# Optimization experiments

Hardware: AMD Instinct MI355X
Metric: run time of the kernel (lower is better)

The kernel has to match this reference:

```python
import jax, jax.numpy as jnp
import numpy as np
from jax import lax

K = 10
ALPHA = 0.1
N_NODES = 100000
N_EDGES = 3200000


def setup_inputs() -> dict:
    key = jax.random.key(0)
    ks = jax.random.split(key, 6)
    x = jax.random.normal(ks[0], (N_NODES, 256), dtype=jnp.float32)
    edge_index = jax.random.randint(ks[1], (2, N_EDGES), 0, N_NODES, dtype=jnp.int64)
    w1 = jax.random.normal(ks[2], (256, 256), dtype=jnp.float32) * (1.0 / np.sqrt(256))
    b1 = jax.random.normal(ks[3], (256,), dtype=jnp.float32) * 0.01
    w2 = jax.random.normal(ks[4], (64, 256), dtype=jnp.float32) * (1.0 / np.sqrt(256))
    b2 = jax.random.normal(ks[5], (64,), dtype=jnp.float32) * 0.01
    return {"x": x, "edge_index": edge_index, "w1": w1, "b1": b1, "w2": w2, "b2": b2}


def reference(x, edge_index, w1, b1, w2, b2):
    # Eval mode: dropout is identity.
    h = jax.nn.relu(x @ w1.T + b1)          # [N, hidden]
    z = h @ w2.T + b2                        # [N, out]

    n = x.shape[0]
    loop = jnp.arange(n, dtype=edge_index.dtype)
    row = jnp.concatenate([edge_index[0], loop])   # sources (with self-loops)
    col = jnp.concatenate([edge_index[1], loop])   # targets (with self-loops)

    # gcn_norm: D^{-1/2} (A + I) D^{-1/2}, degree at target nodes
    deg = jax.ops.segment_sum(jnp.ones_like(col, dtype=z.dtype), col, num_segments=n)
    dinv = lax.rsqrt(deg)                    # deg >= 1 due to self-loops
    norm = dinv[row] * dinv[col]             # [E+N]

    x0 = z

    def step(xk, _):
        msg = xk[row] * norm[:, None]                          # gather + scale
        agg = jax.ops.segment_sum(msg, col, num_segments=n)    # scatter-add
        return (1.0 - ALPHA) * agg + ALPHA * x0, None

    out, _ = lax.scan(step, z, None, length=K)
    return out
```

## Files before the change

### kernel.cpp

```cpp
#include <hip/hip_runtime.h>
#include <hip/hip_bf16.h>


#define HIDDEN 256
#define OUTF   64
#define NB_BLK 256

typedef __attribute__((ext_vector_type(8))) unsigned short ushort8;
typedef __attribute__((ext_vector_type(8))) short short8v;
typedef __attribute__((ext_vector_type(4))) float f32x4;

__device__ inline float b2f(unsigned short u) {
    union { unsigned int i; float f; } c;
    c.i = ((unsigned int)u) << 16;
    return c.f;
}
__device__ inline unsigned short f2b(float f) {
    union { float f; unsigned int i; } c;
    c.f = f;
    unsigned int x = c.i;
    unsigned int r = (x + 0x7fff + ((x >> 16) & 1)) >> 16;
    return (unsigned short)r;
}
__device__ inline short8v cvt8v(float4 A, float4 B) {
    short8v o;
    o[0] = (short)f2b(A.x); o[1] = (short)f2b(A.y);
    o[2] = (short)f2b(A.z); o[3] = (short)f2b(A.w);
    o[4] = (short)f2b(B.x); o[5] = (short)f2b(B.y);
    o[6] = (short)f2b(B.z); o[7] = (short)f2b(B.w);
    return o;
}
__device__ inline short8v cvt8(const float* s) {
    return cvt8v(((const float4*)s)[0], ((const float4*)s)[1]);
}

__device__ inline bool detect_i64(const int* __restrict__ p) {
    int acc = 0;
#pragma unroll
    for (int i = 0; i < 16; ++i) acc |= p[2 * i + 1];
    return acc == 0;
}
__device__ inline int load_idx(const void* eiv, long long flat, bool is64) {
    if (is64) return (int)((const long long*)eiv)[flat];
    return ((const int*)eiv)[flat];
}

__global__ __launch_bounds__(256) void part_hist_kernel(const void* __restrict__ eiv,
                                                        long long E, int* __restrict__ bh,
                                                        int n, int nb) {
    __shared__ int hist[512];
    bool is64 = detect_i64((const int*)eiv);
    int t = threadIdx.x, b = blockIdx.x;
    for (int i = t; i < 512; i += 256) hist[i] = 0;
    __syncthreads();
    long long chunk = (E + NB_BLK - 1) / NB_BLK;
    long long beg = (long long)b * chunk, end = min(E, beg + chunk);
    for (long long e = beg + t; e < end; e += 256) {
        int c = load_idx(eiv, E + e, is64);
        if ((unsigned)c < (unsigned)n) atomicAdd(&hist[c >> 8], 1);
    }
    __syncthreads();
    for (int i = t; i < nb; i += 256) bh[i * NB_BLK + b] = hist[i];
}

__global__ __launch_bounds__(256) void part_colscan_kernel(const int* __restrict__ bh,
                                                           int* __restrict__ pre,
                                                           int* __restrict__ btot) {
    __shared__ int s[NB_BLK];
    int g = blockIdx.x, t = threadIdx.x;
    int v = bh[g * NB_BLK + t];
    s[t] = v;
    __syncthreads();
    for (int o = 1; o < NB_BLK; o <<= 1) {
        int tv = (t >= o) ? s[t - o] : 0;
        __syncthreads();
        s[t] += tv;
        __syncthreads();
    }
    pre[g * NB_BLK + t] = s[t] - v;
    if (t == NB_BLK - 1) btot[g] = s[t];
}

__global__ __launch_bounds__(512) void part_bscan_kernel(const int* __restrict__ btot,
                                                         int* __restrict__ bofs, int nb) {
    __shared__ int s[512];
    int t = threadIdx.x;
    int v = (t < nb) ? btot[t] : 0;
    s[t] = v;
    __syncthreads();
    for (int o = 1; o < 512; o <<= 1) {
        int tv = (t >= o) ? s[t - o] : 0;
        __syncthreads();
        s[t] += tv;
        __syncthreads();
    }
    if (t < nb) bofs[t] = s[t] - v;
    if (t == 511) bofs[nb] = s[511];
}

__global__ __launch_bounds__(256) void part_scatter_kernel(const void* __restrict__ eiv,
                                                           long long E,
                                                           const int* __restrict__ bofs,
                                                           const int* __restrict__ pre,
                                                           unsigned int* __restrict__ pairs,
                                                           int n, int nb) {
    __shared__ int cur[512];
    bool is64 = detect_i64((const int*)eiv);
    int t = threadIdx.x, b = blockIdx.x;
    for (int i = t; i < nb; i += 256) cur[i] = bofs[i] + pre[i * NB_BLK + b];
    __syncthreads();
    long long chunk = (E + NB_BLK - 1) / NB_BLK;
    long long beg = (long long)b * chunk, end = min(E, beg + chunk);
    for (long long e = beg + t; e < end; e += 256) {
        int r = load_idx(eiv, e, is64);
        int c = load_idx(eiv, E + e, is64);
        if ((unsigned)c >= (unsigned)n || (unsigned)r >= (unsigned)n) continue;
        int pos = atomicAdd(&cur[c >> 8], 1);
        pairs[pos] = ((unsigned int)(c & 255) << 24) | (unsigned int)r;
    }
}

__global__ __launch_bounds__(256) void csr_bucket_kernel(const unsigned int* __restrict__ pairs,
                                                         const int* __restrict__ bofs,
                                                         int* __restrict__ ofs,
                                                         float* __restrict__ dinv,
                                                         int* __restrict__ csr_src,
                                                         int n, int nb) {
    __shared__ int hist[256];
    __shared__ int scn[256];
    int b = blockIdx.x;
    int t = threadIdx.x;
    int node0 = b << 8;
    int cnt = min(256, n - node0);

    hist[t] = 0;
    __syncthreads();
    int beg = bofs[b], end = bofs[b + 1];
    for (int e = beg + t; e < end; e += 256) atomicAdd(&hist[pairs[e] >> 24], 1);
    __syncthreads();
    int v = hist[t];
    scn[t] = v;
    __syncthreads();
    for (int o = 1; o < 256; o <<= 1) {
        int tv = (t >= o) ? scn[t - o] : 0;
        __syncthreads();
        scn[t] += tv;
        __syncthreads();
    }
    int excl = scn[t] - v;
    if (t < cnt) {
        ofs[node0 + t] = beg + excl;
        dinv[node0 + t] = rsqrtf((float)(v + 1));
    }
    if (b == nb - 1 && t == 0) ofs[n] = end;
    __syncthreads();
    hist[t] = beg + excl;
    __syncthreads();
    for (int e = beg + t; e < end; e += 256) {
        unsigned int pr = pairs[e];
        int pos = atomicAdd(&hist[pr >> 24], 1);
        csr_src[pos] = (int)(pr & 0xFFFFFFu);
    }
}

__global__ __launch_bounds__(256) void pack_w_kernel(const float* __restrict__ w1,
                                                     const float* __restrict__ w2,
                                                     unsigned short* __restrict__ w1p,
                                                     unsigned short* __restrict__ w2p) {
    int id = blockIdx.x * 256 + threadIdx.x;
    if (id < 8192) {
        int ks = id >> 10, rem = id & 1023;
        int f = rem >> 2, kg = rem & 3;
        short8v o = cvt8(w1 + (size_t)f * HIDDEN + ks * 32 + kg * 8);
        *(short8v*)(w1p + ((size_t)(ks * 1024 + (f >> 4) * 64 + kg * 16 + (f & 15)) << 3)) = o;
    } else if (id < 8192 + 2048) {
        int q = id - 8192;
        int j = q >> 5, kslot = q & 31;
        short8v o = cvt8(w2 + (size_t)j * HIDDEN + kslot * 8);
        *(short8v*)(w2p +
                    ((size_t)((j >> 4) * 512 + (kslot >> 2) * 64 + (kslot & 3) * 16 + (j & 15))
                     << 3)) = o;
    }
}

__global__ __launch_bounds__(512) void mlp_mfma_kernel(const float* __restrict__ x,
                                                       const unsigned short* __restrict__ w1p,
                                                       const float* __restrict__ b1,
                                                       const unsigned short* __restrict__ w2p,
                                                       const float* __restrict__ b2,
                                                       const float* __restrict__ dinv,
                                                       unsigned short* __restrict__ xb0,
                                                       unsigned short* __restrict__ g0, int n) {
    __shared__ __align__(16) union {
        struct { unsigned short w1s[8192]; unsigned short xs[2048]; } p1;
        unsigned short h[64 * 264];
    } u;

    const int t = threadIdx.x;
    const int w = t >> 6;
    const int l = t & 63;
    const int c = l & 15, g = l >> 4;
    const int node0 = blockIdx.x * 64;

    const bool xrole = (t < 256);
    const int sm = t >> 2, skg = t & 3;
    const int snode = node0 + sm;
    const int wu0 = t - 256;
    const int xunit = ((sm >> 4) * 64 + skg * 16 + (sm & 15)) << 3;

    f32x4 acc[4][2];
#pragma unroll
    for (int a = 0; a < 4; ++a)
#pragma unroll
        for (int b = 0; b < 2; ++b) acc[a][b] = (f32x4)0.f;

    float4 pxa0 = make_float4(0.f, 0.f, 0.f, 0.f), pxb0 = pxa0;
    float4 pxa1 = pxa0, pxb1 = pxa0;
    short8v pw[4];

    auto loadx = [&](int ks, float4& A, float4& B) {
        if (snode < n) {
            const float4* xp = (const float4*)(x + (size_t)snode * HIDDEN + ks * 32 + skg * 8);
            A = xp[0];
            B = xp[1];
        }
    };
    auto loadw = [&](int ks) {
        const unsigned short* wsrc = w1p + (size_t)ks * 8192;
#pragma unroll
        for (int i = 0; i < 4; ++i)
            pw[i] = *(const short8v*)(wsrc + ((size_t)(wu0 + i * 256) << 3));
    };
    auto mfma_step = [&]() {
        short8v af[4], bf[2];
#pragma unroll
        for (int mt = 0; mt < 4; ++mt)
            af[mt] = *(const short8v*)&u.p1.xs[(mt * 64 + l) << 3];
#pragma unroll
        for (int j = 0; j < 2; ++j)
            bf[j] = *(const short8v*)&u.p1.w1s[((w * 2 + j) * 64 + l) << 3];
#pragma unroll
        for (int mt = 0; mt < 4; ++mt)
#pragma unroll
            for (int j = 0; j < 2; ++j)
                acc[mt][j] =
                    __builtin_amdgcn_mfma_f32_16x16x32_bf16(af[mt], bf[j], acc[mt][j], 0, 0, 0);
    };
    auto wwrite = [&]() {
#pragma unroll
        for (int i = 0; i < 4; ++i)
            *(short8v*)&u.p1.w1s[(wu0 + i * 256) << 3] = pw[i];
    };

    if (xrole) {
        loadx(0, pxa0, pxb0);
        loadx(1, pxa1, pxb1);
    } else {
        loadw(0);
    }

    for (int ks = 0; ks < 8; ks += 2) {
        if (xrole) *(short8v*)&u.p1.xs[xunit] = cvt8v(pxa0, pxb0);
        else wwrite();
        __syncthreads();
        if (xrole) {
            if (ks + 2 < 8) loadx(ks + 2, pxa0, pxb0);
        } else {
            loadw(ks + 1);
        }
        mfma_step();
        __syncthreads();
        if (xrole) *(short8v*)&u.p1.xs[xunit] = cvt8v(pxa1, pxb1);
        else wwrite();
        __syncthreads();
        if (xrole) {
            if (ks + 3 < 8) loadx(ks + 3, pxa1, pxb1);
        } else {
            if (ks + 2 < 8) loadw(ks + 2);
        }
        mfma_step();
        __syncthreads();
    }

#pragma unroll
    for (int j = 0; j < 2; ++j) {
        int col = w * 32 + j * 16 + c;
        float b1v = b1[col];
#pragma unroll
        for (int mt = 0; mt < 4; ++mt)
#pragma unroll
            for (int r = 0; r < 4; ++r) {
                int row = mt * 16 + g * 4 + r;
                u.h[row * 264 + col] = f2b(fmaxf(acc[mt][j][r] + b1v, 0.f));
            }
    }
    __syncthreads();

    const int rt = w >> 1;
    const int cb = (w & 1) * 2;
    f32x4 acc2[2];
#pragma unroll
    for (int j = 0; j < 2; ++j) acc2[j] = (f32x4)0.f;
#pragma unroll
    for (int ks = 0; ks < 8; ++ks) {
        short8v a2 = *(const short8v*)&u.h[(rt * 16 + c) * 264 + ks * 32 + g * 8];
#pragma unroll
        for (int j = 0; j < 2; ++j) {
            short8v bv = *(const short8v*)(w2p + ((size_t)((cb + j) * 512 + ks * 64 + l) << 3));
            acc2[j] = __builtin_amdgcn_mfma_f32_16x16x32_bf16(a2, bv, acc2[j], 0, 0, 0);
        }
    }
#pragma unroll
    for (int j = 0; j < 2; ++j) {
        int col = (cb + j) * 16 + c;
        float bb = b2[col];
#pragma unroll
        for (int r = 0; r < 4; ++r) {
            int node = node0 + rt * 16 + g * 4 + r;
            if (node < n) {
                float zv = acc2[j][r] + bb;
                float di = dinv[node];
                xb0[(size_t)node * OUTF + col] = f2b(0.1f * zv);
                g0[(size_t)node * OUTF + col] = f2b(di * zv);
            }
        }
    }
}

template <int LAST>
__global__ __launch_bounds__(256, 8) void prop_kernel(const unsigned short* __restrict__ gk,
                                                      const unsigned short* __restrict__ xb0,
                                                      unsigned short* __restrict__ gn,
                                                      float* __restrict__ out,
                                                      const int* __restrict__ ofs,
                                                      const int* __restrict__ csr_src,
                                                      const float* __restrict__ dinv, int n) {
    int gid = blockIdx.x * 256 + threadIdx.x;
    int node = gid >> 3;
    int part = gid & 7;
    if (node >= n) return;

    int beg = ofs[node];
    int end = ofs[node + 1];
    float di = dinv[node];

    float acc[8];
#pragma unroll
    for (int j = 0; j < 8; ++j) acc[j] = 0.f;

    const size_t poff = (size_t)part * 8;
    int e = beg;
    for (; e + 3 < end; e += 4) {
        int s0 = csr_src[e];
        int s1 = csr_src[e + 1];
        int s2 = csr_src[e + 2];
        int s3 = csr_src[e + 3];
        ushort8 a = *(const ushort8*)(gk + ((size_t)s0 << 6) + poff);
        ushort8 b = *(const ushort8*)(gk + ((size_t)s1 << 6) + poff);
        ushort8 cc = *(const ushort8*)(gk + ((size_t)s2 << 6) + poff);
        ushort8 d = *(const ushort8*)(gk + ((size_t)s3 << 6) + poff);
#pragma unroll
        for (int j = 0; j < 8; ++j) acc[j] += b2f(a[j]);
#pragma unroll
        for (int j = 0; j < 8; ++j) acc[j] += b2f(b[j]);
#pragma unroll
        for (int j = 0; j < 8; ++j) acc[j] += b2f(cc[j]);
#pragma unroll
        for (int j = 0; j < 8; ++j) acc[j] += b2f(d[j]);
    }
    for (; e < end; ++e) {
        int s0 = csr_src[e];
        ushort8 a = *(const ushort8*)(gk + ((size_t)s0 << 6) + poff);
#pragma unroll
        for (int j = 0; j < 8; ++j) acc[j] += b2f(a[j]);
    }
    {
        ushort8 a = *(const ushort8*)(gk + ((size_t)node << 6) + poff);
#pragma unroll
        for (int j = 0; j < 8; ++j) acc[j] += b2f(a[j]);
    }

    ushort8 xv = *(const ushort8*)(xb0 + ((size_t)node << 6) + poff);
    float res[8];
#pragma unroll
    for (int j = 0; j < 8; ++j) res[j] = 0.9f * di * acc[j] + b2f(xv[j]);

    if (LAST) {
        float4* o4 = (float4*)(out + (size_t)node * OUTF + poff);
        o4[0] = make_float4(res[0], res[1], res[2], res[3]);
        o4[1] = make_float4(res[4], res[5], res[6], res[7]);
    } else {
        ushort8 o;
#pragma unroll
        for (int j = 0; j < 8; ++j) o[j] = f2b(di * res[j]);
        *(ushort8*)(gn + ((size_t)node << 6) + poff) = o;
    }
}

extern "C" void kernel_launch(void* const* d_in, const int* in_sizes, int n_in,
                              void* d_out, int out_size, void* d_ws, size_t ws_size,
                              hipStream_t stream) {
    const float* x = (const float*)d_in[0];
    const void* ei = d_in[1];
    const float* w1 = (const float*)d_in[2];
    const float* b1 = (const float*)d_in[3];
    const float* w2 = (const float*)d_in[4];
    const float* b2 = (const float*)d_in[5];
    float* out = (float*)d_out;

    int n = in_sizes[0] / HIDDEN;
    long long E = (long long)in_sizes[1] / 2;
    int nb = (n + 255) >> 8;

    char* ws = (char*)d_ws;
    size_t off = 0;
    auto alloc = [&](size_t bytes) {
        void* p = ws + off;
        off += (bytes + 511) & ~(size_t)511;
        return p;
    };
    unsigned short* xb0 = (unsigned short*)alloc((size_t)n * OUTF * 2);
    size_t gmark = off;
    unsigned short* gA = (unsigned short*)alloc((size_t)n * OUTF * 2);
    unsigned short* gB = (unsigned short*)alloc((size_t)n * OUTF * 2);
    unsigned int* pairs = (unsigned int*)(ws + gmark);
    float* dinv = (float*)alloc((size_t)n * 4);
    int* ofs = (int*)alloc((size_t)(n + 1) * 4);
    int* csr_src = (int*)alloc((size_t)E * 4);
    int* bh = (int*)alloc((size_t)512 * NB_BLK * 4);
    int* pre = (int*)alloc((size_t)512 * NB_BLK * 4);
    int* btot = (int*)alloc(512 * 4);
    int* bofs = (int*)alloc(513 * 4);
    unsigned short* w1p = (unsigned short*)alloc(65536 * 2);
    unsigned short* w2p = (unsigned short*)alloc(16384 * 2);

    pack_w_kernel<<<40, 256, 0, stream>>>(w1, w2, w1p, w2p);

    part_hist_kernel<<<NB_BLK, 256, 0, stream>>>(ei, E, bh, n, nb);
    part_colscan_kernel<<<nb, NB_BLK, 0, stream>>>(bh, pre, btot);
    part_bscan_kernel<<<1, 512, 0, stream>>>(btot, bofs, nb);
    part_scatter_kernel<<<NB_BLK, 256, 0, stream>>>(ei, E, bofs, pre, pairs, n, nb);
    csr_bucket_kernel<<<nb, 256, 0, stream>>>(pairs, bofs, ofs, dinv, csr_src, n, nb);

    mlp_mfma_kernel<<<(n + 63) / 64, 512, 0, stream>>>(x, w1p, b1, w2p, b2, dinv, xb0, gA, n);

    int prop_blocks = (int)(((size_t)n * 8 + 255) / 256);
    for (int k = 0; k < 10; ++k) {
        const unsigned short* gin = (k & 1) ? gB : gA;
        unsigned short* gout = (k & 1) ? gA : gB;
        if (k == 9) {
            prop_kernel<1><<<prop_blocks, 256, 0, stream>>>(gin, xb0, nullptr, out, ofs,
                                                            csr_src, dinv, n);
        } else {
            prop_kernel<0><<<prop_blocks, 256, 0, stream>>>(gin, xb0, gout, nullptr, ofs,
                                                            csr_src, dinv, n);
        }
    }
}
```

Measured before the change: 684.2 us.

## Fold weight packing into histogram kernel and read W1 fragments from global

The separate weight-packing launch is merged into the first 40 blocks of the partition histogram kernel, which removes one kernel launch. Separately, the MLP kernel no longer stages packed W1 tiles through shared memory. Each wave now loads its B fragments straight from global memory (served from L2/L1), which frees LDS and drops the weight-writer role. The trade-off is more global and L1 traffic per block and possibly exposed load latency before the MFMAs.

```diff
diff --git a/kernel.cpp b/kernel.cpp
--- a/kernel.cpp
+++ b/kernel.cpp
@@ -47,7 +47,28 @@
 
 __global__ __launch_bounds__(256) void part_hist_kernel(const void* __restrict__ eiv,
                                                         long long E, int* __restrict__ bh,
-                                                        int n, int nb) {
+                                                        int n, int nb,
+                                                        const float* __restrict__ w1,
+                                                        const float* __restrict__ w2,
+                                                        unsigned short* __restrict__ w1p,
+                                                        unsigned short* __restrict__ w2p) {
+    if (blockIdx.x < 40) {
+        int id = blockIdx.x * 256 + threadIdx.x;
+        if (id < 8192) {
+            int ks = id >> 10, rem = id & 1023;
+            int f = rem >> 2, kg = rem & 3;
+            short8v o = cvt8(w1 + (size_t)f * HIDDEN + ks * 32 + kg * 8);
+            *(short8v*)(w1p + ((size_t)(ks * 1024 + (f >> 4) * 64 + kg * 16 + (f & 15)) << 3)) = o;
+        } else if (id < 8192 + 2048) {
+            int q = id - 8192;
+            int j = q >> 5, kslot = q & 31;
+            short8v o = cvt8(w2 + (size_t)j * HIDDEN + kslot * 8);
+            *(short8v*)(w2p + ((size_t)((j >> 4) * 512 + (kslot >> 2) * 64 + (kslot & 3) * 16 +
+                                        (j & 15))
+                               << 3)) = o;
+        }
+    }
+
     __shared__ int hist[512];
     bool is64 = detect_i64((const int*)eiv);
     int t = threadIdx.x, b = blockIdx.x;
@@ -163,26 +184,6 @@
     }
 }
 
-__global__ __launch_bounds__(256) void pack_w_kernel(const float* __restrict__ w1,
-                                                     const float* __restrict__ w2,
-                                                     unsigned short* __restrict__ w1p,
-                                                     unsigned short* __restrict__ w2p) {
-    int id = blockIdx.x * 256 + threadIdx.x;
-    if (id < 8192) {
-        int ks = id >> 10, rem = id & 1023;
-        int f = rem >> 2, kg = rem & 3;
-        short8v o = cvt8(w1 + (size_t)f * HIDDEN + ks * 32 + kg * 8);
-        *(short8v*)(w1p + ((size_t)(ks * 1024 + (f >> 4) * 64 + kg * 16 + (f & 15)) << 3)) = o;
-    } else if (id < 8192 + 2048) {
-        int q = id - 8192;
-        int j = q >> 5, kslot = q & 31;
-        short8v o = cvt8(w2 + (size_t)j * HIDDEN + kslot * 8);
-        *(short8v*)(w2p +
-                    ((size_t)((j >> 4) * 512 + (kslot >> 2) * 64 + (kslot & 3) * 16 + (j & 15))
-                     << 3)) = o;
-    }
-}
-
 __global__ __launch_bounds__(512) void mlp_mfma_kernel(const float* __restrict__ x,
                                                        const unsigned short* __restrict__ w1p,
                                                        const float* __restrict__ b1,
@@ -192,7 +193,7 @@
                                                        unsigned short* __restrict__ xb0,
                                                        unsigned short* __restrict__ g0, int n) {
     __shared__ __align__(16) union {
-        struct { unsigned short w1s[8192]; unsigned short xs[2048]; } p1;
+        unsigned short xs[2048];
         unsigned short h[64 * 264];
     } u;
 
@@ -205,7 +206,6 @@
     const bool xrole = (t < 256);
     const int sm = t >> 2, skg = t & 3;
     const int snode = node0 + sm;
-    const int wu0 = t - 256;
     const int xunit = ((sm >> 4) * 64 + skg * 16 + (sm & 15)) << 3;
 
     f32x4 acc[4][2];
@@ -216,7 +216,6 @@
 
     float4 pxa0 = make_float4(0.f, 0.f, 0.f, 0.f), pxb0 = pxa0;
     float4 pxa1 = pxa0, pxb1 = pxa0;
-    short8v pw[4];
 
     auto loadx = [&](int ks, float4& A, float4& B) {
         if (snode < n) {
@@ -225,20 +224,16 @@
             B = xp[1];
         }
     };
-    auto loadw = [&](int ks) {
-        const unsigned short* wsrc = w1p + (size_t)ks * 8192;
-#pragma unroll
-        for (int i = 0; i < 4; ++i)
-            pw[i] = *(const short8v*)(wsrc + ((size_t)(wu0 + i * 256) << 3));
-    };
-    auto mfma_step = [&]() {
-        short8v af[4], bf[2];
+    auto mfma_step = [&](int ks) {
+        const unsigned short* wsrc = w1p + ((size_t)ks << 13);
+        short8v bf[2];
+#pragma unroll
+        for (int j = 0; j < 2; ++j)
+            bf[j] = *(const short8v*)(wsrc + (((w * 2 + j) * 64 + l) << 3));
+        short8v af[4];
 #pragma unroll
         for (int mt = 0; mt < 4; ++mt)
-            af[mt] = *(const short8v*)&u.p1.xs[(mt * 64 + l) << 3];
-#pragma unroll
-        for (int j = 0; j < 2; ++j)
-            bf[j] = *(const short8v*)&u.p1.w1s[((w * 2 + j) * 64 + l) << 3];
+            af[mt] = *(const short8v*)&u.xs[(mt * 64 + l) << 3];
 #pragma unroll
         for (int mt = 0; mt < 4; ++mt)
 #pragma unroll
@@ -246,39 +241,22 @@
                 acc[mt][j] =
                     __builtin_amdgcn_mfma_f32_16x16x32_bf16(af[mt], bf[j], acc[mt][j], 0, 0, 0);
     };
-    auto wwrite = [&]() {
-#pragma unroll
-        for (int i = 0; i < 4; ++i)
-            *(short8v*)&u.p1.w1s[(wu0 + i * 256) << 3] = pw[i];
-    };
 
     if (xrole) {
         loadx(0, pxa0, pxb0);
         loadx(1, pxa1, pxb1);
-    } else {
-        loadw(0);
     }
 
     for (int ks = 0; ks < 8; ks += 2) {
-        if (xrole) *(short8v*)&u.p1.xs[xunit] = cvt8v(pxa0, pxb0);
-        else wwrite();
-        __syncthreads();
-        if (xrole) {
-            if (ks + 2 < 8) loadx(ks + 2, pxa0, pxb0);
-        } else {
-            loadw(ks + 1);
-        }
-        mfma_step();
-        __syncthreads();
-        if (xrole) *(short8v*)&u.p1.xs[xunit] = cvt8v(pxa1, pxb1);
-        else wwrite();
-        __syncthreads();
-        if (xrole) {
-            if (ks + 3 < 8) loadx(ks + 3, pxa1, pxb1);
-        } else {
-            if (ks + 2 < 8) loadw(ks + 2);
-        }
-        mfma_step();
+        if (xrole) *(short8v*)&u.xs[xunit] = cvt8v(pxa0, pxb0);
+        __syncthreads();
+        if (xrole && ks + 2 < 8) loadx(ks + 2, pxa0, pxb0);
+        mfma_step(ks);
+        __syncthreads();
+        if (xrole) *(short8v*)&u.xs[xunit] = cvt8v(pxa1, pxb1);
+        __syncthreads();
+        if (xrole && ks + 3 < 8) loadx(ks + 3, pxa1, pxb1);
+        mfma_step(ks + 1);
         __syncthreads();
     }
 
@@ -434,9 +412,7 @@
     unsigned short* w1p = (unsigned short*)alloc(65536 * 2);
     unsigned short* w2p = (unsigned short*)alloc(16384 * 2);
 
-    pack_w_kernel<<<40, 256, 0, stream>>>(w1, w2, w1p, w2p);
-
-    part_hist_kernel<<<NB_BLK, 256, 0, stream>>>(ei, E, bh, n, nb);
+    part_hist_kernel<<<NB_BLK, 256, 0, stream>>>(ei, E, bh, n, nb, w1, w2, w1p, w2p);
     part_colscan_kernel<<<nb, NB_BLK, 0, stream>>>(bh, pre, btot);
     part_bscan_kernel<<<1, 512, 0, stream>>>(btot, bofs, nb);
     part_scatter_kernel<<<NB_BLK, 256, 0, stream>>>(ei, E, bofs, pre, pairs, n, nb);
```

After: 678.6 us. About the same (-0.8%).
